# Kernel tuning notes

Hardware: AMD Instinct MI355X
Metric: run time of the kernel (lower is better)

## Reference

```python
import jax, jax.numpy as jnp
import numpy as np

BN_EPS = 1e-5
NN_CHUNK = 1024  # unknown points processed per distance-matrix tile


def _batch_ids(cnt, total):
    # contiguous per-batch layout -> batch id of each point via cumsum/searchsorted
    return jnp.searchsorted(jnp.cumsum(cnt), jnp.arange(total), side='right')


def three_nn(unknown, known, ub_id, kb_id):
    """Ragged brute-force 3-NN. Returns (squared dists [N,3], global idx [N,3])."""
    N = unknown.shape[0]
    nchunk = N // NN_CHUNK
    u = unknown.reshape(nchunk, NN_CHUNK, 3)
    ub = ub_id.reshape(nchunk, NN_CHUNK)

    def body(args):
        uc, bc = args
        d2 = jnp.sum((uc[:, None, :] - known[None, :, :]) ** 2, axis=-1)  # [chunk, M]
        d2 = jnp.where(bc[:, None] == kb_id[None, :], d2, jnp.inf)  # mask cross-batch pairs
        neg_d, idx = jax.lax.top_k(-d2, 3)
        return -neg_d, idx

    d2, idx = jax.lax.map(body, (u, ub))
    return d2.reshape(N, 3), idx.reshape(N, 3)


def three_interpolate(known_feats, idx, weight):
    # gather [N,3,C] then inverse-distance weighted sum -> [N,C]
    gathered = known_feats[idx]  # [N,3,C]
    return jnp.einsum('nkc,nk->nc', gathered, weight)


def conv_bn_relu(x, W, gamma, beta):
    # 1x1 Conv2d over [1,C,N,1] == pointwise matmul; BN (training stats) over points
    h = x @ W.T  # [N, C_out]
    mean = jnp.mean(h, axis=0)
    var = jnp.mean((h - mean) ** 2, axis=0)  # biased, as torch BN normalization
    h = (h - mean) * jax.lax.rsqrt(var + BN_EPS) * gamma + beta
    return jax.nn.relu(h)


def setup_inputs() -> dict:
    key = jax.random.key(0)
    ks = jax.random.split(key, 10)
    B, Nper, Mper, C1, C2 = 4, 16384, 4096, 128, 256
    N, M = B * Nper, B * Mper
    unknown = jax.random.normal(ks[0], (N, 3), jnp.float32) * 10.0
    known = jax.random.normal(ks[1], (M, 3), jnp.float32) * 10.0
    unknown_feats = jax.random.normal(ks[2], (N, C1), jnp.float32)
    known_feats = jax.random.normal(ks[3], (M, C2), jnp.float32)
    unknown_batch_cnt = jnp.full((B,), Nper, jnp.int32)
    known_batch_cnt = jnp.full((B,), Mper, jnp.int32)
    Cin = C1 + C2  # 384
    W1 = jax.random.normal(ks[4], (256, Cin), jnp.float32) * (1.0 / np.sqrt(Cin))
    W2 = jax.random.normal(ks[5], (256, 256), jnp.float32) * (1.0 / np.sqrt(256))
    g1 = jnp.ones((256,), jnp.float32); b1 = jnp.zeros((256,), jnp.float32)
    g2 = jnp.ones((256,), jnp.float32); b2 = jnp.zeros((256,), jnp.float32)
    return {"unknown": unknown, "unknown_batch_cnt": unknown_batch_cnt,
            "known": known, "known_batch_cnt": known_batch_cnt,
            "unknown_feats": unknown_feats, "known_feats": known_feats,
            "W1": W1, "g1": g1, "b1": b1, "W2": W2, "g2": g2, "b2": b2}


def reference(unknown, unknown_batch_cnt, known, known_batch_cnt,
              unknown_feats, known_feats, W1, g1, b1, W2, g2, b2):
    ub_id = _batch_ids(unknown_batch_cnt, unknown.shape[0])
    kb_id = _batch_ids(known_batch_cnt, known.shape[0])
    dist, idx = three_nn(unknown, known, ub_id, kb_id)  # squared dists, as CUDA kernel
    dist_recip = 1.0 / (dist + 1e-8)
    weight = dist_recip / jnp.sum(dist_recip, axis=-1, keepdims=True)
    interpolated = three_interpolate(known_feats, idx, weight)  # [N, C2]
    new_features = jnp.concatenate([interpolated, unknown_feats], axis=1)  # [N, C2+C1]
    new_features = conv_bn_relu(new_features, W1, g1, b1)
    new_features = conv_bn_relu(new_features, W2, g2, b2)
    return new_features  # [N, 256]
```

## Files before the change

kernel.cpp:

```cpp
#include <hip/hip_runtime.h>
#include <math.h>

typedef __attribute__((ext_vector_type(8))) short short8;
typedef __attribute__((ext_vector_type(4))) float f32x4;

#define INF 3.0e38f

__device__ __forceinline__ unsigned short f2bf(float x) {
    union { float f; unsigned u; } v; v.f = x;
    unsigned r = v.u + 0x7FFF + ((v.u >> 16) & 1);
    return (unsigned short)(r >> 16);
}

__global__ __launch_bounds__(256) void knn3_kernel(
    const float* __restrict__ unk, const float* __restrict__ kn,
    const int* __restrict__ ucnt, const int* __restrict__ kcnt,
    int B, int N, float* __restrict__ wgt, int* __restrict__ idxo)
{
    __shared__ float4 kxyz[1024];
    __shared__ float md[4][64][3];
    __shared__ int   mi[4][64][3];

    int tid = threadIdx.x;
    int s = tid >> 6;
    int lane = tid & 63;
    int pbase = blockIdx.x * 64;
    int p = pbase + lane;

    int cum = 0, bb = 0;
    for (int i = 0; i < B; i++) { int c = ucnt[i]; if (pbase >= cum) bb = i; cum += c; }
    int kstart = 0;
    for (int i = 0; i < bb; i++) kstart += kcnt[i];
    int kend = kstart + kcnt[bb];

    float ux = unk[p * 3 + 0], uy = unk[p * 3 + 1], uz = unk[p * 3 + 2];

    float d0 = INF, d1 = INF, d2 = INF;
    int   i0 = 0, i1 = 0, i2 = 0;

    auto ins = [&](float e, int gj) {
        bool cA = e < d0;
        bool cB = e < d1;
        bool cC = e < d2;
        int ni0 = cA ? gj : i0;
        int ni1 = cA ? i0 : (cB ? gj : i1);
        int ni2 = cB ? i1 : (cC ? gj : i2);
        float nd0 = fminf(e, d0);
        float nd1 = fminf(fmaxf(e, d0), d1);
        float nd2 = fminf(d2, fmaxf(e, d1));
        d0 = nd0; d1 = nd1; d2 = nd2;
        i0 = ni0; i1 = ni1; i2 = ni2;
    };

    for (int t0g = kstart; t0g < kend; t0g += 1024) {
        int cnt = min(1024, kend - t0g);
        __syncthreads();
        for (int f = tid; f < cnt * 3; f += 256) {
            int pt = f / 3, c = f - pt * 3;
            ((float*)&kxyz[pt])[c] = kn[(size_t)(t0g + pt) * 3 + c];
        }
        __syncthreads();

        int qlen = cnt >> 2;
        int base = s * qlen;
        for (int i = 0; i < qlen; i += 4) {
            float4 a = kxyz[base + i];
            float4 b4 = kxyz[base + i + 1];
            float4 c4 = kxyz[base + i + 2];
            float4 d4 = kxyz[base + i + 3];
            float ax = ux - a.x,  ay = uy - a.y,  az = uz - a.z;
            float bx = ux - b4.x, by = uy - b4.y, bz = uz - b4.z;
            float cx = ux - c4.x, cy = uy - c4.y, cz = uz - c4.z;
            float dx = ux - d4.x, dy = uy - d4.y, dz = uz - d4.z;
            float e0 = ax * ax + ay * ay + az * az;
            float e1 = bx * bx + by * by + bz * bz;
            float e2 = cx * cx + cy * cy + cz * cz;
            float e3 = dx * dx + dy * dy + dz * dz;
            int gj = t0g + base + i;
            ins(e0, gj + 0);
            ins(e1, gj + 1);
            ins(e2, gj + 2);
            ins(e3, gj + 3);
        }
    }

    md[s][lane][0] = d0; md[s][lane][1] = d1; md[s][lane][2] = d2;
    mi[s][lane][0] = i0; mi[s][lane][1] = i1; mi[s][lane][2] = i2;
    __syncthreads();

    if (tid < 64) {
        unsigned long long s0 = ~0ULL, s1 = ~0ULL, s2 = ~0ULL;
        auto insK = [&](unsigned long long k) {
            bool c0 = k < s0;
            unsigned long long t0 = c0 ? k : s0;
            unsigned long long t1 = c0 ? s0 : k;
            bool c1 = t1 < s1;
            unsigned long long u0 = c1 ? t1 : s1;
            unsigned long long u1 = c1 ? s1 : t1;
            s0 = t0; s1 = u0;
            s2 = u1 < s2 ? u1 : s2;
        };
#pragma unroll
        for (int qq = 0; qq < 4; qq++)
#pragma unroll
            for (int kk = 0; kk < 3; kk++)
                insK(((unsigned long long)__float_as_uint(md[qq][tid][kk]) << 32)
                     | (unsigned)mi[qq][tid][kk]);

        float dd0 = __uint_as_float((unsigned)(s0 >> 32));
        float dd1 = __uint_as_float((unsigned)(s1 >> 32));
        float dd2 = __uint_as_float((unsigned)(s2 >> 32));
        float r0 = 1.0f / (dd0 + 1e-8f);
        float r1 = 1.0f / (dd1 + 1e-8f);
        float r2 = 1.0f / (dd2 + 1e-8f);
        float rs = 1.0f / (r0 + r1 + r2);
        int pp = pbase + tid;
        wgt[pp * 3 + 0] = r0 * rs;
        wgt[pp * 3 + 1] = r1 * rs;
        wgt[pp * 3 + 2] = r2 * rs;
        idxo[pp * 3 + 0] = (int)(unsigned)s0;
        idxo[pp * 3 + 1] = (int)(unsigned)s1;
        idxo[pp * 3 + 2] = (int)(unsigned)s2;
    }
}

__global__ __launch_bounds__(256) void build_a1_kernel(
    const float* __restrict__ wgt, const int* __restrict__ idxv,
    const float* __restrict__ kfeat, const float* __restrict__ ufeat,
    unsigned short* __restrict__ A1, int N)
{
    int t = blockIdx.x * 256 + threadIdx.x;
    int p = t >> 6, c4 = t & 63;
    if (p >= N) return;
    float w0 = wgt[p * 3 + 0], w1 = wgt[p * 3 + 1], w2 = wgt[p * 3 + 2];
    int j0 = idxv[p * 3 + 0], j1 = idxv[p * 3 + 1], j2 = idxv[p * 3 + 2];
    float4 v0 = ((const float4*)(kfeat + (size_t)j0 * 256))[c4];
    float4 v1 = ((const float4*)(kfeat + (size_t)j1 * 256))[c4];
    float4 v2 = ((const float4*)(kfeat + (size_t)j2 * 256))[c4];
    ushort4 ob;
    ob.x = f2bf(v0.x * w0 + v1.x * w1 + v2.x * w2);
    ob.y = f2bf(v0.y * w0 + v1.y * w1 + v2.y * w2);
    ob.z = f2bf(v0.z * w0 + v1.z * w1 + v2.z * w2);
    ob.w = f2bf(v0.w * w0 + v1.w * w1 + v2.w * w2);
    *(ushort4*)(A1 + (size_t)p * 384 + c4 * 4) = ob;
    float2 u = ((const float2*)(ufeat + (size_t)p * 128))[c4];
    ushort2 ub; ub.x = f2bf(u.x); ub.y = f2bf(u.y);
    *(ushort2*)(A1 + (size_t)p * 384 + 256 + c4 * 2) = ub;
}

__global__ __launch_bounds__(256) void wconv_kernel(
    const float* __restrict__ W1, const float* __restrict__ W2,
    unsigned short* __restrict__ W1b, unsigned short* __restrict__ W2b,
    int n1, int n2)
{
    int i = blockIdx.x * 256 + threadIdx.x;
    if (i < n1) W1b[i] = f2bf(W1[i]);
    int j = i - n1;
    if (j >= 0 && j < n2) W2b[j] = f2bf(W2[j]);
}

template <int K, int MODE>
__global__ __launch_bounds__(256) void gemm_bf16_kernel(
    const void* __restrict__ Av, const unsigned short* __restrict__ W,
    const float* __restrict__ scale, const float* __restrict__ shift,
    float* __restrict__ C, float* __restrict__ gsum, float* __restrict__ gsq)
{
    __shared__ unsigned short As[128 * 40];
    __shared__ unsigned short Bs[128 * 40];
    __shared__ float colsum[128];
    __shared__ float colsq[128];

    int tid = threadIdx.x;
    int w = tid >> 6, lane = tid & 63;
    int r = w >> 1, cq = w & 1;
    int m16 = lane & 15, q = lane >> 4;
    int bm = blockIdx.x * 128, bn = blockIdx.y * 128;

    f32x4 acc[4][4];
#pragma unroll
    for (int i = 0; i < 4; i++)
#pragma unroll
        for (int j = 0; j < 4; j++) acc[i][j] = (f32x4){0.f, 0.f, 0.f, 0.f};

#pragma unroll
    for (int k0 = 0; k0 < K; k0 += 32) {
        __syncthreads();
#pragma unroll
        for (int i = 0; i < 2; i++) {
            int id = tid + i * 256;
            int row = id >> 2, kc = (id & 3) * 8;
            if (MODE == 0) {
                *(short8*)&As[row * 40 + kc] =
                    *(const short8*)((const unsigned short*)Av +
                                     (size_t)(bm + row) * K + k0 + kc);
            } else {
                const float* Af = (const float*)Av;
                float4 v0 = *(const float4*)(Af + (size_t)(bm + row) * K + k0 + kc);
                float4 v1 = *(const float4*)(Af + (size_t)(bm + row) * K + k0 + kc + 4);
                float4 s0 = *(const float4*)(scale + k0 + kc);
                float4 s1 = *(const float4*)(scale + k0 + kc + 4);
                float4 t0 = *(const float4*)(shift + k0 + kc);
                float4 t1 = *(const float4*)(shift + k0 + kc + 4);
                ushort4 o0, o1;
                o0.x = f2bf(fmaxf(v0.x * s0.x + t0.x, 0.f));
                o0.y = f2bf(fmaxf(v0.y * s0.y + t0.y, 0.f));
                o0.z = f2bf(fmaxf(v0.z * s0.z + t0.z, 0.f));
                o0.w = f2bf(fmaxf(v0.w * s0.w + t0.w, 0.f));
                o1.x = f2bf(fmaxf(v1.x * s1.x + t1.x, 0.f));
                o1.y = f2bf(fmaxf(v1.y * s1.y + t1.y, 0.f));
                o1.z = f2bf(fmaxf(v1.z * s1.z + t1.z, 0.f));
                o1.w = f2bf(fmaxf(v1.w * s1.w + t1.w, 0.f));
                *(ushort4*)&As[row * 40 + kc] = o0;
                *(ushort4*)&As[row * 40 + kc + 4] = o1;
            }
            *(short8*)&Bs[row * 40 + kc] =
                *(const short8*)(W + (size_t)(bn + row) * K + k0 + kc);
        }
        __syncthreads();

        short8 af[4], bf[4];
#pragma unroll
        for (int sub = 0; sub < 4; sub++) {
            af[sub] = *(const short8*)&As[(r * 64 + sub * 16 + m16) * 40 + q * 8];
            bf[sub] = *(const short8*)&Bs[(cq * 64 + sub * 16 + m16) * 40 + q * 8];
        }
#pragma unroll
        for (int sm = 0; sm < 4; sm++)
#pragma unroll
            for (int sn = 0; sn < 4; sn++)
                acc[sm][sn] = __builtin_amdgcn_mfma_f32_16x16x32_bf16(
                    af[sm], bf[sn], acc[sm][sn], 0, 0, 0);
    }

    int row0 = bm + r * 64 + q * 4;
    int col0 = bn + cq * 64 + m16;
#pragma unroll
    for (int sm = 0; sm < 4; sm++)
#pragma unroll
        for (int sn = 0; sn < 4; sn++) {
            f32x4 v = acc[sm][sn];
#pragma unroll
            for (int reg = 0; reg < 4; reg++)
                C[(size_t)(row0 + sm * 16 + reg) * 256 + col0 + sn * 16] = v[reg];
        }

    __syncthreads();
    if (tid < 128) { colsum[tid] = 0.f; colsq[tid] = 0.f; }
    __syncthreads();
#pragma unroll
    for (int sn = 0; sn < 4; sn++) {
        float sacc = 0.f, qacc = 0.f;
#pragma unroll
        for (int sm = 0; sm < 4; sm++) {
            f32x4 v = acc[sm][sn];
#pragma unroll
            for (int reg = 0; reg < 4; reg++) {
                sacc += v[reg];
                qacc += v[reg] * v[reg];
            }
        }
        int lc = cq * 64 + sn * 16 + m16;
        atomicAdd(&colsum[lc], sacc);
        atomicAdd(&colsq[lc], qacc);
    }
    __syncthreads();
    if (tid < 128) {
        atomicAdd(&gsum[bn + tid], colsum[tid]);
        atomicAdd(&gsq[bn + tid], colsq[tid]);
    }
}

__global__ void bn_finalize_kernel(
    const float* __restrict__ sum, const float* __restrict__ sumsq,
    const float* __restrict__ g, const float* __restrict__ bta, float invN,
    float* __restrict__ scale, float* __restrict__ shift)
{
    int c = threadIdx.x;
    float mean = sum[c] * invN;
    float var = sumsq[c] * invN - mean * mean;
    float sc = g[c] * rsqrtf(var + 1e-5f);
    scale[c] = sc;
    shift[c] = bta[c] - mean * sc;
}

__global__ __launch_bounds__(256) void final_act_kernel(
    const float* __restrict__ h2, const float* __restrict__ scale,
    const float* __restrict__ shift, float* __restrict__ out, int total4)
{
    int i = blockIdx.x * 256 + threadIdx.x;
    if (i >= total4) return;
    int c4 = i & 63;
    float4 v = ((const float4*)h2)[i];
    float4 s = ((const float4*)scale)[c4];
    float4 t = ((const float4*)shift)[c4];
    float4 o;
    o.x = fmaxf(v.x * s.x + t.x, 0.0f);
    o.y = fmaxf(v.y * s.y + t.y, 0.0f);
    o.z = fmaxf(v.z * s.z + t.z, 0.0f);
    o.w = fmaxf(v.w * s.w + t.w, 0.0f);
    ((float4*)out)[i] = o;
}

extern "C" void kernel_launch(void* const* d_in, const int* in_sizes, int n_in,
                              void* d_out, int out_size, void* d_ws, size_t ws_size,
                              hipStream_t stream)
{
    const float* unknown = (const float*)d_in[0];
    const int*   ucnt    = (const int*)d_in[1];
    const float* known   = (const float*)d_in[2];
    const int*   kcnt    = (const int*)d_in[3];
    const float* ufeat   = (const float*)d_in[4];
    const float* kfeat   = (const float*)d_in[5];
    const float* W1      = (const float*)d_in[6];
    const float* g1      = (const float*)d_in[7];
    const float* b1      = (const float*)d_in[8];
    const float* W2      = (const float*)d_in[9];
    const float* g2      = (const float*)d_in[10];
    const float* b2      = (const float*)d_in[11];

    int N = in_sizes[0] / 3;
    int B = in_sizes[1];

    char* ws = (char*)d_ws;
    size_t off = 0;
    float* wgt = (float*)(ws + off);            off += (size_t)N * 3 * 4;
    int*   idxb = (int*)(ws + off);             off += (size_t)N * 3 * 4;
    float* stats = (float*)(ws + off);          off += 8 * 256 * 4;
    float* sum1 = stats,         *sq1 = stats + 256;
    float* scale1 = stats + 512, *shift1 = stats + 768;
    float* sum2 = stats + 1024,  *sq2 = stats + 1280;
    float* scale2 = stats + 1536, *shift2 = stats + 1792;
    unsigned short* W1b = (unsigned short*)(ws + off);  off += 256 * 384 * 2;
    unsigned short* W2b = (unsigned short*)(ws + off);  off += 256 * 256 * 2;
    off = (off + 255) & ~(size_t)255;
    unsigned short* A1 = (unsigned short*)(ws + off);
    float* h2 = (float*)(ws + off);
    float* h1 = (float*)d_out;

    hipMemsetAsync(stats, 0, 8 * 256 * 4, stream);

    knn3_kernel<<<N / 64, 256, 0, stream>>>(unknown, known, ucnt, kcnt,
                                            B, N, wgt, idxb);
    build_a1_kernel<<<N / 4, 256, 0, stream>>>(wgt, idxb, kfeat, ufeat, A1, N);
    wconv_kernel<<<(256 * 384 + 256 * 256 + 255) / 256, 256, 0, stream>>>(
        W1, W2, W1b, W2b, 256 * 384, 256 * 256);
    gemm_bf16_kernel<384, 0><<<dim3(N / 128, 2), 256, 0, stream>>>(
        A1, W1b, nullptr, nullptr, h1, sum1, sq1);
    bn_finalize_kernel<<<1, 256, 0, stream>>>(sum1, sq1, g1, b1, 1.0f / N,
                                              scale1, shift1);
    gemm_bf16_kernel<256, 1><<<dim3(N / 128, 2), 256, 0, stream>>>(
        h1, W2b, scale1, shift1, h2, sum2, sq2);
    bn_finalize_kernel<<<1, 256, 0, stream>>>(sum2, sq2, g2, b2, 1.0f / N,
                                              scale2, shift2);
    final_act_kernel<<<N / 4, 256, 0, stream>>>(h2, scale2, shift2,
                                                (float*)d_out, N * 64);
}
```

Baseline: 412.7 us.

## Replace brute-force 3-NN with per-batch uniform grid search

Replaces the brute-force per-batch 3-NN scan with a uniform 32^3 grid per batch. It adds a bounding-box pass, a cell histogram, a prefix scan, a scatter of known points into cells, and then searches outward in cubic shells around each query's cell until the third-best distance is inside the bound. This removes the O(N*M) distance work in exchange for several small launches, atomics, and divergent per-thread shell loops. The key packing of (dist, index) keeps tie-breaking by the lower index.

```diff
diff --git a/kernel.cpp b/kernel.cpp
--- a/kernel.cpp
+++ b/kernel.cpp
@@ -5,6 +5,9 @@
 typedef __attribute__((ext_vector_type(4))) float f32x4;
 
 #define INF 3.0e38f
+#define NCELL1 32
+#define NCELL3 32768
+#define NCHUNK 512
 
 __device__ __forceinline__ unsigned short f2bf(float x) {
     union { float f; unsigned u; } v; v.f = x;
@@ -12,116 +15,211 @@
     return (unsigned short)(r >> 16);
 }
 
-__global__ __launch_bounds__(256) void knn3_kernel(
-    const float* __restrict__ unk, const float* __restrict__ kn,
-    const int* __restrict__ ucnt, const int* __restrict__ kcnt,
-    int B, int N, float* __restrict__ wgt, int* __restrict__ idxo)
-{
-    __shared__ float4 kxyz[1024];
-    __shared__ float md[4][64][3];
-    __shared__ int   mi[4][64][3];
-
+__device__ __forceinline__ int cellc(float v, float bmin, float invh) {
+    int c = (int)floorf((v - bmin) * invh);
+    return min(NCELL1 - 1, max(0, c));
+}
+
+__global__ __launch_bounds__(256) void bbox_kernel(
+    const float* __restrict__ kn, const int* __restrict__ kcnt, int B,
+    float* __restrict__ bbox)
+{
+    int b = blockIdx.x;
+    int kstart = 0;
+    for (int i = 0; i < b; i++) kstart += kcnt[i];
+    int kend = kstart + kcnt[b];
+    float mn[3] = {INF, INF, INF}, mx[3] = {-INF, -INF, -INF};
+    for (int i = kstart + threadIdx.x; i < kend; i += 256) {
+        for (int c = 0; c < 3; c++) {
+            float v = kn[(size_t)i * 3 + c];
+            mn[c] = fminf(mn[c], v);
+            mx[c] = fmaxf(mx[c], v);
+        }
+    }
+    __shared__ float smn[3][256], smx[3][256];
+    for (int c = 0; c < 3; c++) { smn[c][threadIdx.x] = mn[c]; smx[c][threadIdx.x] = mx[c]; }
+    __syncthreads();
+    for (int off = 128; off > 0; off >>= 1) {
+        if (threadIdx.x < off)
+            for (int c = 0; c < 3; c++) {
+                smn[c][threadIdx.x] = fminf(smn[c][threadIdx.x], smn[c][threadIdx.x + off]);
+                smx[c][threadIdx.x] = fmaxf(smx[c][threadIdx.x], smx[c][threadIdx.x + off]);
+            }
+        __syncthreads();
+    }
+    if (threadIdx.x == 0)
+        for (int c = 0; c < 3; c++) {
+            bbox[b * 6 + c] = smn[c][0];
+            bbox[b * 6 + 3 + c] = smx[c][0];
+        }
+}
+
+__global__ __launch_bounds__(256) void hist_kernel(
+    const float* __restrict__ kn, const int* __restrict__ kcnt, int B, int M,
+    const float* __restrict__ bbox, int* __restrict__ counts)
+{
+    int i = blockIdx.x * 256 + threadIdx.x;
+    if (i >= M) return;
+    int cum = 0, b = 0;
+    for (int j = 0; j < B; j++) { int c = kcnt[j]; if (i >= cum) b = j; cum += c; }
+    float x = kn[(size_t)i * 3 + 0], y = kn[(size_t)i * 3 + 1], z = kn[(size_t)i * 3 + 2];
+    float bx = bbox[b * 6 + 0], by = bbox[b * 6 + 1], bz = bbox[b * 6 + 2];
+    float ix = (float)NCELL1 / fmaxf(bbox[b * 6 + 3] - bx, 1e-6f);
+    float iy = (float)NCELL1 / fmaxf(bbox[b * 6 + 4] - by, 1e-6f);
+    float iz = (float)NCELL1 / fmaxf(bbox[b * 6 + 5] - bz, 1e-6f);
+    int cx = cellc(x, bx, ix), cy = cellc(y, by, iy), cz = cellc(z, bz, iz);
+    int cid = (b << 15) + (cz << 10) + (cy << 5) + cx;
+    atomicAdd(&counts[cid], 1);
+}
+
+__global__ __launch_bounds__(256) void scan1_kernel(
+    const int* __restrict__ counts, int* __restrict__ excl, int* __restrict__ bsum)
+{
+    __shared__ int sh[256];
     int tid = threadIdx.x;
-    int s = tid >> 6;
-    int lane = tid & 63;
-    int pbase = blockIdx.x * 64;
-    int p = pbase + lane;
-
-    int cum = 0, bb = 0;
-    for (int i = 0; i < B; i++) { int c = ucnt[i]; if (pbase >= cum) bb = i; cum += c; }
-    int kstart = 0;
-    for (int i = 0; i < bb; i++) kstart += kcnt[i];
-    int kend = kstart + kcnt[bb];
-
-    float ux = unk[p * 3 + 0], uy = unk[p * 3 + 1], uz = unk[p * 3 + 2];
-
-    float d0 = INF, d1 = INF, d2 = INF;
-    int   i0 = 0, i1 = 0, i2 = 0;
-
-    auto ins = [&](float e, int gj) {
-        bool cA = e < d0;
-        bool cB = e < d1;
-        bool cC = e < d2;
-        int ni0 = cA ? gj : i0;
-        int ni1 = cA ? i0 : (cB ? gj : i1);
-        int ni2 = cB ? i1 : (cC ? gj : i2);
-        float nd0 = fminf(e, d0);
-        float nd1 = fminf(fmaxf(e, d0), d1);
-        float nd2 = fminf(d2, fmaxf(e, d1));
-        d0 = nd0; d1 = nd1; d2 = nd2;
-        i0 = ni0; i1 = ni1; i2 = ni2;
+    int g = blockIdx.x * 256 + tid;
+    int v = counts[g];
+    sh[tid] = v;
+    __syncthreads();
+    int x = v;
+    for (int off = 1; off < 256; off <<= 1) {
+        int y = (tid >= off) ? sh[tid - off] : 0;
+        __syncthreads();
+        x += y;
+        sh[tid] = x;
+        __syncthreads();
+    }
+    excl[g] = x - v;
+    if (tid == 255) bsum[blockIdx.x] = x;
+}
+
+__global__ __launch_bounds__(512) void scan2_kernel(
+    const int* __restrict__ bsum, int* __restrict__ bbase, int* __restrict__ fs)
+{
+    __shared__ int sh[512];
+    int tid = threadIdx.x;
+    int v = bsum[tid];
+    sh[tid] = v;
+    __syncthreads();
+    int x = v;
+    for (int off = 1; off < 512; off <<= 1) {
+        int y = (tid >= off) ? sh[tid - off] : 0;
+        __syncthreads();
+        x += y;
+        sh[tid] = x;
+        __syncthreads();
+    }
+    bbase[tid] = x - v;
+    if (tid == 511) fs[NCHUNK * 256] = x;
+}
+
+__global__ __launch_bounds__(256) void fixup_kernel(
+    const int* __restrict__ excl, const int* __restrict__ bbase, int* __restrict__ fs)
+{
+    int g = blockIdx.x * 256 + threadIdx.x;
+    fs[g] = excl[g] + bbase[g >> 8];
+}
+
+__global__ __launch_bounds__(256) void scatter_kernel(
+    const float* __restrict__ kn, const int* __restrict__ kcnt, int B, int M,
+    const float* __restrict__ bbox, const int* __restrict__ fs,
+    int* __restrict__ cursor, float4* __restrict__ pts)
+{
+    int i = blockIdx.x * 256 + threadIdx.x;
+    if (i >= M) return;
+    int cum = 0, b = 0;
+    for (int j = 0; j < B; j++) { int c = kcnt[j]; if (i >= cum) b = j; cum += c; }
+    float x = kn[(size_t)i * 3 + 0], y = kn[(size_t)i * 3 + 1], z = kn[(size_t)i * 3 + 2];
+    float bx = bbox[b * 6 + 0], by = bbox[b * 6 + 1], bz = bbox[b * 6 + 2];
+    float ix = (float)NCELL1 / fmaxf(bbox[b * 6 + 3] - bx, 1e-6f);
+    float iy = (float)NCELL1 / fmaxf(bbox[b * 6 + 4] - by, 1e-6f);
+    float iz = (float)NCELL1 / fmaxf(bbox[b * 6 + 5] - bz, 1e-6f);
+    int cx = cellc(x, bx, ix), cy = cellc(y, by, iy), cz = cellc(z, bz, iz);
+    int cid = (b << 15) + (cz << 10) + (cy << 5) + cx;
+    int slot = atomicAdd(&cursor[cid], 1);
+    float4 r; r.x = x; r.y = y; r.z = z; r.w = __int_as_float(i);
+    pts[fs[cid] + slot] = r;
+}
+
+__global__ __launch_bounds__(256) void knn_grid_kernel(
+    const float* __restrict__ unk, const int* __restrict__ ucnt, int B, int N,
+    const float* __restrict__ bbox, const int* __restrict__ fs,
+    const float4* __restrict__ pts,
+    float* __restrict__ wgt, int* __restrict__ idxo)
+{
+    int p = blockIdx.x * 256 + threadIdx.x;
+    if (p >= N) return;
+    int cum = 0, b = 0;
+    for (int j = 0; j < B; j++) { int c = ucnt[j]; if (p >= cum) b = j; cum += c; }
+
+    float qx = unk[(size_t)p * 3 + 0], qy = unk[(size_t)p * 3 + 1], qz = unk[(size_t)p * 3 + 2];
+    float bx = bbox[b * 6 + 0], by = bbox[b * 6 + 1], bz = bbox[b * 6 + 2];
+    float ex = fmaxf(bbox[b * 6 + 3] - bx, 1e-6f);
+    float ey = fmaxf(bbox[b * 6 + 4] - by, 1e-6f);
+    float ez = fmaxf(bbox[b * 6 + 5] - bz, 1e-6f);
+    float ix = (float)NCELL1 / ex, iy = (float)NCELL1 / ey, iz = (float)NCELL1 / ez;
+    float hmin = fminf(fminf(ex, ey), ez) * (1.0f / NCELL1);
+    int cx = cellc(qx, bx, ix), cy = cellc(qy, by, iy), cz = cellc(qz, bz, iz);
+    int cbase = b << 15;
+
+    unsigned long long s0 = ~0ULL, s1 = ~0ULL, s2 = ~0ULL;
+    auto insK = [&](unsigned long long k) {
+        bool c0 = k < s0;
+        unsigned long long t0 = c0 ? k : s0;
+        unsigned long long t1 = c0 ? s0 : k;
+        bool c1 = t1 < s1;
+        unsigned long long u0 = c1 ? t1 : s1;
+        unsigned long long u1 = c1 ? s1 : t1;
+        s0 = t0; s1 = u0;
+        s2 = u1 < s2 ? u1 : s2;
     };
 
-    for (int t0g = kstart; t0g < kend; t0g += 1024) {
-        int cnt = min(1024, kend - t0g);
-        __syncthreads();
-        for (int f = tid; f < cnt * 3; f += 256) {
-            int pt = f / 3, c = f - pt * 3;
-            ((float*)&kxyz[pt])[c] = kn[(size_t)(t0g + pt) * 3 + c];
-        }
-        __syncthreads();
-
-        int qlen = cnt >> 2;
-        int base = s * qlen;
-        for (int i = 0; i < qlen; i += 4) {
-            float4 a = kxyz[base + i];
-            float4 b4 = kxyz[base + i + 1];
-            float4 c4 = kxyz[base + i + 2];
-            float4 d4 = kxyz[base + i + 3];
-            float ax = ux - a.x,  ay = uy - a.y,  az = uz - a.z;
-            float bx = ux - b4.x, by = uy - b4.y, bz = uz - b4.z;
-            float cx = ux - c4.x, cy = uy - c4.y, cz = uz - c4.z;
-            float dx = ux - d4.x, dy = uy - d4.y, dz = uz - d4.z;
-            float e0 = ax * ax + ay * ay + az * az;
-            float e1 = bx * bx + by * by + bz * bz;
-            float e2 = cx * cx + cy * cy + cz * cz;
-            float e3 = dx * dx + dy * dy + dz * dz;
-            int gj = t0g + base + i;
-            ins(e0, gj + 0);
-            ins(e1, gj + 1);
-            ins(e2, gj + 2);
-            ins(e3, gj + 3);
-        }
-    }
-
-    md[s][lane][0] = d0; md[s][lane][1] = d1; md[s][lane][2] = d2;
-    mi[s][lane][0] = i0; mi[s][lane][1] = i1; mi[s][lane][2] = i2;
-    __syncthreads();
-
-    if (tid < 64) {
-        unsigned long long s0 = ~0ULL, s1 = ~0ULL, s2 = ~0ULL;
-        auto insK = [&](unsigned long long k) {
-            bool c0 = k < s0;
-            unsigned long long t0 = c0 ? k : s0;
-            unsigned long long t1 = c0 ? s0 : k;
-            bool c1 = t1 < s1;
-            unsigned long long u0 = c1 ? t1 : s1;
-            unsigned long long u1 = c1 ? s1 : t1;
-            s0 = t0; s1 = u0;
-            s2 = u1 < s2 ? u1 : s2;
-        };
-#pragma unroll
-        for (int qq = 0; qq < 4; qq++)
-#pragma unroll
-            for (int kk = 0; kk < 3; kk++)
-                insK(((unsigned long long)__float_as_uint(md[qq][tid][kk]) << 32)
-                     | (unsigned)mi[qq][tid][kk]);
-
-        float dd0 = __uint_as_float((unsigned)(s0 >> 32));
-        float dd1 = __uint_as_float((unsigned)(s1 >> 32));
-        float dd2 = __uint_as_float((unsigned)(s2 >> 32));
-        float r0 = 1.0f / (dd0 + 1e-8f);
-        float r1 = 1.0f / (dd1 + 1e-8f);
-        float r2 = 1.0f / (dd2 + 1e-8f);
-        float rs = 1.0f / (r0 + r1 + r2);
-        int pp = pbase + tid;
-        wgt[pp * 3 + 0] = r0 * rs;
-        wgt[pp * 3 + 1] = r1 * rs;
-        wgt[pp * 3 + 2] = r2 * rs;
-        idxo[pp * 3 + 0] = (int)(unsigned)s0;
-        idxo[pp * 3 + 1] = (int)(unsigned)s1;
-        idxo[pp * 3 + 2] = (int)(unsigned)s2;
-    }
+    for (int rho = 0; rho < NCELL1; rho++) {
+        if (rho >= 2) {
+            float bnd = (float)(rho - 1) * hmin;
+            float d2v = __uint_as_float((unsigned)(s2 >> 32));
+            if (d2v < bnd * bnd) break;
+        }
+        int zlo = max(cz - rho, 0), zhi = min(cz + rho, NCELL1 - 1);
+        for (int z = zlo; z <= zhi; z++) {
+            bool zface = (z == cz - rho) || (z == cz + rho);
+            int ylo = max(cy - rho, 0), yhi = min(cy + rho, NCELL1 - 1);
+            for (int y = ylo; y <= yhi; y++) {
+                bool yface = (y == cy - rho) || (y == cy + rho);
+                int xlo, xhi, xstep;
+                if (zface || yface) { xlo = max(cx - rho, 0); xhi = min(cx + rho, NCELL1 - 1); xstep = 1; }
+                else                { xlo = cx - rho; xhi = cx + rho; xstep = 2 * rho; }
+                for (int x = xlo; x <= xhi; x += xstep) {
+                    if (x < 0 || x > NCELL1 - 1) continue;
+                    int cid = cbase + (z << 10) + (y << 5) + x;
+                    int st = fs[cid], en = fs[cid + 1];
+                    for (int t = st; t < en; t++) {
+                        float4 kp = pts[t];
+                        float dx = qx - kp.x, dy = qy - kp.y, dz = qz - kp.z;
+                        float e = dx * dx + dy * dy + dz * dz;
+                        unsigned long long key =
+                            ((unsigned long long)__float_as_uint(e) << 32)
+                            | (unsigned)__float_as_int(kp.w);
+                        insK(key);
+                    }
+                }
+            }
+        }
+    }
+
+    float d0 = __uint_as_float((unsigned)(s0 >> 32));
+    float d1 = __uint_as_float((unsigned)(s1 >> 32));
+    float d2 = __uint_as_float((unsigned)(s2 >> 32));
+    float r0 = 1.0f / (d0 + 1e-8f);
+    float r1 = 1.0f / (d1 + 1e-8f);
+    float r2 = 1.0f / (d2 + 1e-8f);
+    float rs = 1.0f / (r0 + r1 + r2);
+    wgt[p * 3 + 0] = r0 * rs;
+    wgt[p * 3 + 1] = r1 * rs;
+    wgt[p * 3 + 2] = r2 * rs;
+    idxo[p * 3 + 0] = (int)(unsigned)s0;
+    idxo[p * 3 + 1] = (int)(unsigned)s1;
+    idxo[p * 3 + 2] = (int)(unsigned)s2;
 }
 
 __global__ __launch_bounds__(256) void build_a1_kernel(
@@ -320,6 +418,7 @@
 
     int N = in_sizes[0] / 3;
     int B = in_sizes[1];
+    int M = in_sizes[2] / 3;
 
     char* ws = (char*)d_ws;
     size_t off = 0;
@@ -330,20 +429,38 @@
     float* scale1 = stats + 512, *shift1 = stats + 768;
     float* sum2 = stats + 1024,  *sq2 = stats + 1280;
     float* scale2 = stats + 1536, *shift2 = stats + 1792;
+    float* bbox = (float*)(ws + off);           off += 64 * 4;
     unsigned short* W1b = (unsigned short*)(ws + off);  off += 256 * 384 * 2;
     unsigned short* W2b = (unsigned short*)(ws + off);  off += 256 * 256 * 2;
     off = (off + 255) & ~(size_t)255;
-    unsigned short* A1 = (unsigned short*)(ws + off);
-    float* h2 = (float*)(ws + off);
+
+    char* big = ws + off;
+    int*  counts = (int*)big;
+    int*  cursor = (int*)(big + 512 * 1024);
+    int*  excl   = (int*)(big + 1024 * 1024);
+    int*  fs     = (int*)(big + 1536 * 1024);
+    int*  bsum   = (int*)(big + 2052 * 1024);
+    int*  bbase  = (int*)(big + 2056 * 1024);
+    float4* pts  = (float4*)(big + 2060 * 1024);
+    unsigned short* A1 = (unsigned short*)big;
+    float* h2 = (float*)big;
     float* h1 = (float*)d_out;
 
     hipMemsetAsync(stats, 0, 8 * 256 * 4, stream);
-
-    knn3_kernel<<<N / 64, 256, 0, stream>>>(unknown, known, ucnt, kcnt,
-                                            B, N, wgt, idxb);
-    build_a1_kernel<<<N / 4, 256, 0, stream>>>(wgt, idxb, kfeat, ufeat, A1, N);
+    hipMemsetAsync(counts, 0, 2 * 512 * 1024, stream);
+
+    bbox_kernel<<<B, 256, 0, stream>>>(known, kcnt, B, bbox);
+    hist_kernel<<<(M + 255) / 256, 256, 0, stream>>>(known, kcnt, B, M, bbox, counts);
+    scan1_kernel<<<NCHUNK, 256, 0, stream>>>(counts, excl, bsum);
+    scan2_kernel<<<1, 512, 0, stream>>>(bsum, bbase, fs);
+    fixup_kernel<<<NCHUNK, 256, 0, stream>>>(excl, bbase, fs);
+    scatter_kernel<<<(M + 255) / 256, 256, 0, stream>>>(known, kcnt, B, M, bbox,
+                                                        fs, cursor, pts);
+    knn_grid_kernel<<<N / 256, 256, 0, stream>>>(unknown, ucnt, B, N, bbox, fs,
+                                                 pts, wgt, idxb);
     wconv_kernel<<<(256 * 384 + 256 * 256 + 255) / 256, 256, 0, stream>>>(
         W1, W2, W1b, W2b, 256 * 384, 256 * 256);
+    build_a1_kernel<<<N / 4, 256, 0, stream>>>(wgt, idxb, kfeat, ufeat, A1, N);
     gemm_bf16_kernel<384, 0><<<dim3(N / 128, 2), 256, 0, stream>>>(
         A1, W1b, nullptr, nullptr, h1, sum1, sq1);
     bn_finalize_kernel<<<1, 256, 0, stream>>>(sum1, sq1, g1, b1, 1.0f / N,
```

Result: slower. 1.400 ms (+239.2%).

## Split 3-NN into distance-only threshold pass and filtered index pass

Applied to the files above, without the earlier changes.

The KNN kernel now runs two passes over the known points. The first pass tracks only the three smallest distances, with no index bookkeeping, and merges them across the four wave slices to get a per-point third-nearest threshold. The second pass recomputes distances and does the 64-bit key insertion only for groups of four whose minimum is at or below that threshold. This cuts select and compare work in the hot loop, but it loads and computes every distance twice and adds a branch that may diverge. The weight conversion launch is also moved ahead of the gather launch.

```diff
diff --git a/kernel.cpp b/kernel.cpp
--- a/kernel.cpp
+++ b/kernel.cpp
@@ -12,6 +12,11 @@
     return (unsigned short)(r >> 16);
 }
 
+__device__ __forceinline__ float dist2(float ux, float uy, float uz, float4 k) {
+    float dx = ux - k.x, dy = uy - k.y, dz = uz - k.z;
+    return __builtin_fmaf(dx, dx, __builtin_fmaf(dy, dy, dz * dz));
+}
+
 __global__ __launch_bounds__(256) void knn3_kernel(
     const float* __restrict__ unk, const float* __restrict__ kn,
     const int* __restrict__ ucnt, const int* __restrict__ kcnt,
@@ -19,7 +24,8 @@
 {
     __shared__ float4 kxyz[1024];
     __shared__ float md[4][64][3];
-    __shared__ int   mi[4][64][3];
+    __shared__ float d2g[64];
+    __shared__ unsigned long long mk[4][64][3];
 
     int tid = threadIdx.x;
     int s = tid >> 6;
@@ -36,20 +42,12 @@
     float ux = unk[p * 3 + 0], uy = unk[p * 3 + 1], uz = unk[p * 3 + 2];
 
     float d0 = INF, d1 = INF, d2 = INF;
-    int   i0 = 0, i1 = 0, i2 = 0;
-
-    auto ins = [&](float e, int gj) {
-        bool cA = e < d0;
-        bool cB = e < d1;
-        bool cC = e < d2;
-        int ni0 = cA ? gj : i0;
-        int ni1 = cA ? i0 : (cB ? gj : i1);
-        int ni2 = cB ? i1 : (cC ? gj : i2);
-        float nd0 = fminf(e, d0);
-        float nd1 = fminf(fmaxf(e, d0), d1);
-        float nd2 = fminf(d2, fmaxf(e, d1));
-        d0 = nd0; d1 = nd1; d2 = nd2;
-        i0 = ni0; i1 = ni1; i2 = ni2;
+    auto upd = [&](float e) {
+        float m0 = fmaxf(e, d0);
+        float m1 = fmaxf(e, d1);
+        d0 = fminf(e, d0);
+        d1 = fminf(m0, d1);
+        d2 = fminf(m1, d2);
     };
 
     for (int t0g = kstart; t0g < kend; t0g += 1024) {
@@ -64,48 +62,86 @@
         int qlen = cnt >> 2;
         int base = s * qlen;
         for (int i = 0; i < qlen; i += 4) {
-            float4 a = kxyz[base + i];
-            float4 b4 = kxyz[base + i + 1];
-            float4 c4 = kxyz[base + i + 2];
-            float4 d4 = kxyz[base + i + 3];
-            float ax = ux - a.x,  ay = uy - a.y,  az = uz - a.z;
-            float bx = ux - b4.x, by = uy - b4.y, bz = uz - b4.z;
-            float cx = ux - c4.x, cy = uy - c4.y, cz = uz - c4.z;
-            float dx = ux - d4.x, dy = uy - d4.y, dz = uz - d4.z;
-            float e0 = ax * ax + ay * ay + az * az;
-            float e1 = bx * bx + by * by + bz * bz;
-            float e2 = cx * cx + cy * cy + cz * cz;
-            float e3 = dx * dx + dy * dy + dz * dz;
-            int gj = t0g + base + i;
-            ins(e0, gj + 0);
-            ins(e1, gj + 1);
-            ins(e2, gj + 2);
-            ins(e3, gj + 3);
+            float e0 = dist2(ux, uy, uz, kxyz[base + i]);
+            float e1 = dist2(ux, uy, uz, kxyz[base + i + 1]);
+            float e2 = dist2(ux, uy, uz, kxyz[base + i + 2]);
+            float e3 = dist2(ux, uy, uz, kxyz[base + i + 3]);
+            upd(e0); upd(e1); upd(e2); upd(e3);
         }
     }
 
     md[s][lane][0] = d0; md[s][lane][1] = d1; md[s][lane][2] = d2;
-    mi[s][lane][0] = i0; mi[s][lane][1] = i1; mi[s][lane][2] = i2;
-    __syncthreads();
-
+    __syncthreads();
     if (tid < 64) {
-        unsigned long long s0 = ~0ULL, s1 = ~0ULL, s2 = ~0ULL;
-        auto insK = [&](unsigned long long k) {
-            bool c0 = k < s0;
-            unsigned long long t0 = c0 ? k : s0;
-            unsigned long long t1 = c0 ? s0 : k;
-            bool c1 = t1 < s1;
-            unsigned long long u0 = c1 ? t1 : s1;
-            unsigned long long u1 = c1 ? s1 : t1;
-            s0 = t0; s1 = u0;
-            s2 = u1 < s2 ? u1 : s2;
-        };
+        float v0 = INF, v1 = INF, v2 = INF;
+#pragma unroll
+        for (int w = 0; w < 4; w++)
+#pragma unroll
+            for (int k = 0; k < 3; k++) {
+                float e = md[w][tid][k];
+                float m0 = fmaxf(e, v0);
+                float m1 = fmaxf(e, v1);
+                v0 = fminf(e, v0);
+                v1 = fminf(m0, v1);
+                v2 = fminf(m1, v2);
+            }
+        d2g[tid] = v2;
+    }
+    __syncthreads();
+    float thr = d2g[lane];
+
+    unsigned long long s0 = ~0ULL, s1 = ~0ULL, s2 = ~0ULL;
+    auto insK = [&](unsigned long long k) {
+        bool c0 = k < s0;
+        unsigned long long t0 = c0 ? k : s0;
+        unsigned long long t1 = c0 ? s0 : k;
+        bool c1 = t1 < s1;
+        unsigned long long u0 = c1 ? t1 : s1;
+        unsigned long long u1 = c1 ? s1 : t1;
+        s0 = t0; s1 = u0;
+        s2 = u1 < s2 ? u1 : s2;
+    };
+    auto mkkey = [](float e, int gj) {
+        return ((unsigned long long)__float_as_uint(e) << 32) | (unsigned)gj;
+    };
+
+    for (int t0g = kstart; t0g < kend; t0g += 1024) {
+        int cnt = min(1024, kend - t0g);
+        __syncthreads();
+        for (int f = tid; f < cnt * 3; f += 256) {
+            int pt = f / 3, c = f - pt * 3;
+            ((float*)&kxyz[pt])[c] = kn[(size_t)(t0g + pt) * 3 + c];
+        }
+        __syncthreads();
+
+        int qlen = cnt >> 2;
+        int base = s * qlen;
+        for (int i = 0; i < qlen; i += 4) {
+            float e0 = dist2(ux, uy, uz, kxyz[base + i]);
+            float e1 = dist2(ux, uy, uz, kxyz[base + i + 1]);
+            float e2 = dist2(ux, uy, uz, kxyz[base + i + 2]);
+            float e3 = dist2(ux, uy, uz, kxyz[base + i + 3]);
+            float m4 = fminf(fminf(e0, e1), fminf(e2, e3));
+            if (m4 <= thr) {
+                int gj = t0g + base + i;
+                insK(mkkey(e0, gj + 0));
+                insK(mkkey(e1, gj + 1));
+                insK(mkkey(e2, gj + 2));
+                insK(mkkey(e3, gj + 3));
+            }
+        }
+    }
+
+    mk[s][lane][0] = s0; mk[s][lane][1] = s1; mk[s][lane][2] = s2;
+    __syncthreads();
+
+    if (tid < 64) {
+        s0 = s1 = s2 = ~0ULL;
 #pragma unroll
         for (int qq = 0; qq < 4; qq++)
 #pragma unroll
             for (int kk = 0; kk < 3; kk++)
-                insK(((unsigned long long)__float_as_uint(md[qq][tid][kk]) << 32)
-                     | (unsigned)mi[qq][tid][kk]);
+                insK(mk[qq][tid][kk]);
 
         float dd0 = __uint_as_float((unsigned)(s0 >> 32));
         float dd1 = __uint_as_float((unsigned)(s1 >> 32));
@@ -341,9 +377,9 @@
 
     knn3_kernel<<<N / 64, 256, 0, stream>>>(unknown, known, ucnt, kcnt,
                                             B, N, wgt, idxb);
-    build_a1_kernel<<<N / 4, 256, 0, stream>>>(wgt, idxb, kfeat, ufeat, A1, N);
     wconv_kernel<<<(256 * 384 + 256 * 256 + 255) / 256, 256, 0, stream>>>(
         W1, W2, W1b, W2b, 256 * 384, 256 * 256);
+    build_a1_kernel<<<N / 4, 256, 0, stream>>>(wgt, idxb, kfeat, ufeat, A1, N);
     gemm_bf16_kernel<384, 0><<<dim3(N / 128, 2), 256, 0, stream>>>(
         A1, W1b, nullptr, nullptr, h1, sum1, sq1);
     bn_finalize_kernel<<<1, 256, 0, stream>>>(sum1, sq1, g1, b1, 1.0f / N,
```

Measured after the change: 413.6 us. No clear change (+0.2%).
